# Kernel tuning notes

Measured on AMD Instinct MI355X. Metric: run time of the kernel, lower is better.

Reference implementation:

```python
import jax, jax.numpy as jnp
import numpy as np

S, B, D, H = 1024, 8, 256, 8
DH = D // H
N = S * B
E = 262144
EPS = 1e-5


def setup_inputs():
    key = jax.random.key(0)
    ks = jax.random.split(key, 10)
    g = lambda k, shp, s=0.05: jax.random.normal(k, shp, jnp.float32) * s
    return {
        "x": g(ks[0], (S, B, D), 1.0),
        "condition": g(ks[1], (S, B, 1), 1.0),
        "in_proj_w": g(ks[2], (3 * D, D)),
        "in_proj_b": jnp.zeros((3 * D,), jnp.float32),
        "out_proj_w": g(ks[3], (D, D)),
        "out_proj_b": jnp.zeros((D,), jnp.float32),
        "g1": jnp.ones((D,), jnp.float32), "be1": jnp.zeros((D,), jnp.float32),
        "g2": jnp.ones((D,), jnp.float32), "be2": jnp.zeros((D,), jnp.float32),
        "g3": jnp.ones((D,), jnp.float32), "be3": jnp.zeros((D,), jnp.float32),
        "lin_w": g(ks[4], (D, D)),
        "att_src": g(ks[5], (H, DH)),
        "att_dst": g(ks[6], (H, DH)),
        "gat_bias": jnp.zeros((D,), jnp.float32),
        "w1": g(ks[7], (4 * D, D + 1)),
        "bf1": jnp.zeros((4 * D,), jnp.float32),
        "w2": g(ks[8], (D, 4 * D)),
        "bf2": jnp.zeros((D,), jnp.float32),
        "edge_index": jax.random.randint(ks[9], (2, E), 0, N, jnp.int32),
    }


def _ln(x, g, b):
    m = jnp.mean(x, axis=-1, keepdims=True)
    v = jnp.mean((x - m) ** 2, axis=-1, keepdims=True)
    return (x - m) * jax.lax.rsqrt(v + EPS) * g + b


def _forward(x, condition, in_proj_w, in_proj_b, out_proj_w, out_proj_b,
             g1, be1, g2, be2, g3, be3, lin_w, att_src, att_dst, gat_bias,
             w1, bf1, w2, bf2, edge_index):
    # ---- self-attention (torch MHA, seq-major [S,B,D]) ----
    qkv = jnp.einsum('sbd,ed->sbe', x, in_proj_w) + in_proj_b
    q, k, v = jnp.split(qkv, 3, axis=-1)
    q = q.reshape(S, B, H, DH)
    k = k.reshape(S, B, H, DH)
    v = v.reshape(S, B, H, DH)
    scores = jnp.einsum('sbhd,tbhd->bhst', q, k) / np.float32(np.sqrt(DH))
    a = jax.nn.softmax(scores, axis=-1)
    ctx = jnp.einsum('bhst,tbhd->sbhd', a, v).reshape(S, B, D)
    attn_out = ctx @ out_proj_w.T + out_proj_b
    x1 = _ln(x + attn_out, g1, be1)
    # ---- GATConv over flattened (batch-major) nodes ----
    xr = x1.transpose(1, 0, 2).reshape(N, D)          # node i = b*S + s
    xh = (xr @ lin_w.T).reshape(N, H, DH)
    loops = jnp.arange(N, dtype=edge_index.dtype)     # PyG add_self_loops=True
    src = jnp.concatenate([edge_index[0], loops])
    dst = jnp.concatenate([edge_index[1], loops])
    a_src = jnp.sum(xh * att_src, axis=-1)            # [N,H]
    a_dst = jnp.sum(xh * att_dst, axis=-1)
    e = jax.nn.leaky_relu(a_src[src] + a_dst[dst], 0.2)  # [Et,H]
    m = jax.ops.segment_max(e, dst, num_segments=N)
    ee = jnp.exp(e - m[dst])
    z = jax.ops.segment_sum(ee, dst, num_segments=N)
    alpha = ee / z[dst]
    msg = xh[src] * alpha[:, :, None]                 # [Et,H,DH]
    gout = jax.ops.segment_sum(msg, dst, num_segments=N).reshape(N, D) + gat_bias
    gout = gout.reshape(B, S, D).transpose(1, 0, 2)
    x2 = _ln(x1 + gout, g2, be2)
    # ---- conditioned FFN ----
    xc = jnp.concatenate([x2, condition], axis=-1)    # [S,B,D+1]
    h = jax.nn.relu(xc @ w1.T + bf1)
    f = h @ w2.T + bf2
    return _ln(x2 + f, g3, be3)


def reference(x, condition, in_proj_w, in_proj_b, out_proj_w, out_proj_b,
              g1, be1, g2, be2, g3, be3, lin_w, att_src, att_dst, gat_bias,
              w1, bf1, w2, bf2, edge_index):
    return _forward(x, condition, in_proj_w, in_proj_b, out_proj_w, out_proj_b,
                    g1, be1, g2, be2, g3, be3, lin_w, att_src, att_dst, gat_bias,
                    w1, bf1, w2, bf2, edge_index)
```

## Files before the change

### kernel.cpp

```cpp
#include <hip/hip_runtime.h>
#include <hip/hip_bf16.h>

#define S_ 1024
#define B_ 8
#define D_ 256
#define H_ 8
#define DH_ 32
#define N_ 8192
#define E_ 262144
#define ET_ 270336

typedef unsigned short u16;
typedef float f32x4 __attribute__((ext_vector_type(4)));
typedef __bf16 bf16x8 __attribute__((ext_vector_type(8)));
typedef short s16x4 __attribute__((ext_vector_type(4)));

#define QK_SCALE 0.17677669529663687f

__device__ inline u16 f2bf(float v) {
    unsigned int u = __float_as_uint(v);
    u = (u + 0x7fffu + ((u >> 16) & 1u)) >> 16;
    return (u16)u;
}
__device__ inline float bf2f(u16 u) { return __uint_as_float(((unsigned int)u) << 16); }

__device__ inline unsigned int pack_trunc(float lo, float hi) {
    return __builtin_amdgcn_perm(__float_as_uint(hi), __float_as_uint(lo), 0x07060302u);
}

__device__ inline void gload16(const u16* g, u16* l) {
    __builtin_amdgcn_global_load_lds((const __attribute__((address_space(1))) unsigned int*)g,
                                     (__attribute__((address_space(3))) unsigned int*)l, 16, 0, 0);
}

__device__ inline f32x4 mfma16bf(s16x4 a, s16x4 b, f32x4 c) {
#if __has_builtin(__builtin_amdgcn_mfma_f32_16x16x16bf16_1k)
    return __builtin_amdgcn_mfma_f32_16x16x16bf16_1k(a, b, c, 0, 0, 0);
#else
    asm volatile("v_mfma_f32_16x16x16_bf16 %0, %1, %2, %0" : "+v"(c) : "v"(a), "v"(b));
    return c;
#endif
}

__global__ __launch_bounds__(256) void convert_all(const float* __restrict__ x,  const float* __restrict__ wi,
                                                   const float* __restrict__ wo, const float* __restrict__ wl,
                                                   const float* __restrict__ w1, const float* __restrict__ w2,
                                                   u16* __restrict__ Xbf, u16* __restrict__ Wi, u16* __restrict__ Wo,
                                                   u16* __restrict__ Wl, u16* __restrict__ W1, u16* __restrict__ W2,
                                                   int* __restrict__ count, int* __restrict__ cursor)
{
    const int idx = blockIdx.x * 256 + threadIdx.x;
    const int C0 = 2097152;
    const int C1 = C0 + 196608;
    const int C2 = C1 + 65536;
    const int C3 = C2 + 65536;
    const int C4 = C3 + 294912;
    const int C5 = C4 + 262144;
    const int C6 = C5 + 16384;
    if (idx < C0)      { Xbf[idx] = f2bf(x[idx]); }
    else if (idx < C1) { int i = idx - C0; Wi[i] = f2bf(wi[i]); }
    else if (idx < C2) { int i = idx - C1; Wo[i] = f2bf(wo[i]); }
    else if (idx < C3) { int i = idx - C2; Wl[i] = f2bf(wl[i]); }
    else if (idx < C4) { int i = idx - C3; int r = i / 288, k = i - r * 288;
                         W1[i] = (k < 257) ? f2bf(w1[r * 257 + k]) : (u16)0; }
    else if (idx < C5) { int i = idx - C4; W2[i] = f2bf(w2[i]); }
    else if (idx < C6) { int i = idx - C5; if (i < 8192) count[i] = 0; else cursor[i - 8192] = 0; }
}

template<int BN, int OUTMODE, bool RELU>
__global__ __launch_bounds__(256) void gemm_a16(const u16* __restrict__ A, int lda,
                                                const u16* __restrict__ W, int ldw,
                                                const float* __restrict__ bias,
                                                void* __restrict__ Cv, int ldc, int Ksz)
{
    constexpr int NF = BN / 32;
    __shared__ u16 As[2][128 * 32];
    __shared__ u16 Bs[2][BN * 32];
    const int tid = threadIdx.x;
    const int m0 = blockIdx.y * 128, n0 = blockIdx.x * BN;
    const int lane = tid & 63, w = tid >> 6;
    const int wm = w >> 1, wn = w & 1;
    const int lr = lane & 15, lg = lane >> 4;

    f32x4 acc[4][NF] = {};

    const u16* Ag = A + (size_t)(m0 + (tid >> 2)) * lda + (tid & 3) * 8;
    const u16* Wg = W + (size_t)(n0 + (tid >> 2)) * ldw + (tid & 3) * 8;

    auto stage = [&](int buf, int k0) {
        gload16(Ag + k0,                      &As[buf][tid * 8]);
        gload16(Ag + (size_t)64 * lda + k0,   &As[buf][64 * 32 + tid * 8]);
        gload16(Wg + k0,                      &Bs[buf][tid * 8]);
        if constexpr (BN == 128)
            gload16(Wg + (size_t)64 * ldw + k0, &Bs[buf][64 * 32 + tid * 8]);
    };

    stage(0, 0);
    __syncthreads();
    const int nt = Ksz >> 5;
    int cur = 0;
    for (int kt = 0; kt < nt; ++kt) {
        if (kt + 1 < nt) stage(cur ^ 1, (kt + 1) << 5);
        bf16x8 af[4], bg[NF];
        #pragma unroll
        for (int i = 0; i < 4; ++i)  af[i] = *(const bf16x8*)&As[cur][(wm * 64 + i * 16 + lr) * 32 + lg * 8];
        #pragma unroll
        for (int i = 0; i < NF; ++i) bg[i] = *(const bf16x8*)&Bs[cur][(wn * (BN / 2) + i * 16 + lr) * 32 + lg * 8];
        #pragma unroll
        for (int mi = 0; mi < 4; ++mi)
            #pragma unroll
            for (int ni = 0; ni < NF; ++ni)
                acc[mi][ni] = __builtin_amdgcn_mfma_f32_16x16x32_bf16(af[mi], bg[ni], acc[mi][ni], 0, 0, 0);
        __syncthreads();
        cur ^= 1;
    }
    #pragma unroll
    for (int mi = 0; mi < 4; ++mi)
        #pragma unroll
        for (int ni = 0; ni < NF; ++ni) {
            const int col = n0 + wn * (BN / 2) + ni * 16 + lr;
            const float bv = bias ? bias[col] : 0.f;
            #pragma unroll
            for (int r = 0; r < 4; ++r) {
                const int row = m0 + wm * 64 + mi * 16 + lg * 4 + r;
                float v = acc[mi][ni][r] + bv;
                if (RELU) v = fmaxf(v, 0.f);
                if constexpr (OUTMODE == 1) ((u16*)Cv)[(size_t)row * ldc + col] = f2bf(v);
                else {
                    const int part = col >> 8, hh = (col >> 5) & 7, dh = col & 31;
                    const int ss = row >> 3, bb = row & 7;
                    ((u16*)Cv)[(((size_t)((part * 8 + bb) * 8 + hh)) * 1024 + ss) * 32 + dh] = f2bf(v);
                }
            }
        }
}

template<int MODE>
__global__ __launch_bounds__(512) void gemm_ln(const u16* __restrict__ A, int lda,
                                               const u16* __restrict__ W, int ldw, int Ksz,
                                               const float* __restrict__ bias,
                                               const float* __restrict__ resid,
                                               const float* __restrict__ gamma,
                                               const float* __restrict__ beta,
                                               const float* __restrict__ att_s,
                                               const float* __restrict__ att_d,
                                               float* __restrict__ outf,
                                               u16* __restrict__ outn,
                                               float* __restrict__ asrc,
                                               float* __restrict__ adst)
{
    constexpr int BM = 32;
    __shared__ u16 As[2][BM * 32];
    __shared__ u16 Bs[2][256 * 32];
    __shared__ float2 red[BM][8];
    const int tid = threadIdx.x;
    const int m0 = blockIdx.x * BM;
    const int lane = tid & 63, w = tid >> 6;
    const int rw = w >> 2, cw = w & 3;
    const int lr = lane & 15, lg = lane >> 4;

    f32x4 acc[4] = {};

    auto stage = [&](int buf, int k0) {
        #pragma unroll
        for (int j = 0; j < 2; ++j) {
            const int idx = tid + j * 512;
            gload16(W + (size_t)(idx >> 2) * ldw + (idx & 3) * 8 + k0, &Bs[buf][idx * 8]);
        }
        if (tid < BM * 4)
            gload16(A + (size_t)(m0 + (tid >> 2)) * lda + (tid & 3) * 8 + k0, &As[buf][tid * 8]);
    };
    stage(0, 0);
    __syncthreads();
    const int nt = Ksz >> 5;
    int cur = 0;
    for (int kt = 0; kt < nt; ++kt) {
        if (kt + 1 < nt) stage(cur ^ 1, (kt + 1) << 5);
        bf16x8 af = *(const bf16x8*)&As[cur][(rw * 16 + lr) * 32 + lg * 8];
        bf16x8 bg[4];
        #pragma unroll
        for (int i = 0; i < 4; ++i)  bg[i] = *(const bf16x8*)&Bs[cur][(cw * 64 + i * 16 + lr) * 32 + lg * 8];
        #pragma unroll
        for (int ni = 0; ni < 4; ++ni)
            acc[ni] = __builtin_amdgcn_mfma_f32_16x16x32_bf16(af, bg[ni], acc[ni], 0, 0, 0);
        __syncthreads();
        cur ^= 1;
    }
    int col[4]; float gam[4], bet[4], bv[4], asv[4], adv[4];
    #pragma unroll
    for (int ni = 0; ni < 4; ++ni) {
        col[ni] = cw * 64 + ni * 16 + lr;
        if (MODE != 1) { gam[ni] = gamma[col[ni]]; bet[ni] = beta[col[ni]]; bv[ni] = bias[col[ni]]; }
        else           { asv[ni] = att_s[col[ni]]; adv[ni] = att_d[col[ni]]; }
    }
    #pragma unroll
    for (int r = 0; r < 4; ++r) {
        const int row = rw * 16 + lg * 4 + r;
        const int grow = m0 + row;
        float s1 = 0.f, s2 = 0.f;
        float2 sp0 = {0.f, 0.f}, sp1 = {0.f, 0.f};
        #pragma unroll
        for (int ni = 0; ni < 4; ++ni) {
            float v = acc[ni][r];
            if (MODE != 1) v += bv[ni] + resid[(size_t)grow * 256 + col[ni]];
            acc[ni][r] = v;
            if (MODE == 1) {
                if (ni < 2) { sp0.x += v * asv[ni]; sp0.y += v * adv[ni]; }
                else        { sp1.x += v * asv[ni]; sp1.y += v * adv[ni]; }
            } else { s1 += v; s2 += v * v; }
        }
        #pragma unroll
        for (int msk = 1; msk < 16; msk <<= 1) {
            if (MODE == 1) {
                sp0.x += __shfl_xor(sp0.x, msk, 64); sp0.y += __shfl_xor(sp0.y, msk, 64);
                sp1.x += __shfl_xor(sp1.x, msk, 64); sp1.y += __shfl_xor(sp1.y, msk, 64);
            } else { s1 += __shfl_xor(s1, msk, 64); s2 += __shfl_xor(s2, msk, 64); }
        }
        if (lr == 0) {
            if (MODE == 1) { red[row][cw * 2] = sp0; red[row][cw * 2 + 1] = sp1; }
            else           { red[row][cw] = (float2){s1, s2}; }
        }
    }
    __syncthreads();
    if (MODE == 1) {
        #pragma unroll
        for (int r = 0; r < 4; ++r) {
            const int grow = m0 + rw * 16 + lg * 4 + r;
            #pragma unroll
            for (int ni = 0; ni < 4; ++ni)
                outn[(size_t)grow * 256 + col[ni]] = f2bf(acc[ni][r]);
        }
        for (int idx = tid; idx < BM * 8; idx += 512) {
            const int row = idx >> 3, h = idx & 7;
            asrc[(size_t)(m0 + row) * 8 + h] = red[row][h].x;
            adst[(size_t)(m0 + row) * 8 + h] = red[row][h].y;
        }
    } else {
        #pragma unroll
        for (int r = 0; r < 4; ++r) {
            const int row = rw * 16 + lg * 4 + r;
            const int grow = m0 + row;
            const float2 t0 = red[row][0], t1 = red[row][1], t2 = red[row][2], t3 = red[row][3];
            const float mean = (t0.x + t1.x + t2.x + t3.x) * (1.f / 256.f);
            const float var  = (t0.y + t1.y + t2.y + t3.y) * (1.f / 256.f) - mean * mean;
            const float rs = rsqrtf(var + 1e-5f);
            #pragma unroll
            for (int ni = 0; ni < 4; ++ni) {
                const float o = (acc[ni][r] - mean) * rs * gam[ni] + bet[ni];
                outf[(size_t)grow * 256 + col[ni]] = o;
                if (MODE == 0) {
                    const int node = (grow & 7) * 1024 + (grow >> 3);
                    outn[(size_t)node * 256 + col[ni]] = f2bf(o);
                }
            }
        }
    }
}

__global__ __launch_bounds__(512) void attn_mfma(const u16* __restrict__ qkv, u16* __restrict__ ctx)
{
    const int qt = blockIdx.x, bh = blockIdx.y;
    const int b = bh >> 3, h = bh & 7;
    const int tid = threadIdx.x, lane = tid & 63, w = tid >> 6;
    const int c = lane & 15, g = lane >> 4;

    __shared__ __align__(16) u16 Ks[128][40];
    __shared__ __align__(16) u16 Vt[32][132];

    const size_t plane = (size_t)(b * 8 + h) * 32768;
    const int q0 = qt * 128 + w * 16;
    const bf16x8 qf = *(const bf16x8*)&qkv[plane + (size_t)(q0 + c) * 32 + g * 8];
    const u16* kbase = qkv + 2097152 + plane;

    float m = -1e30f, l = 0.f;
    f32x4 o0 = {}, o1 = {};

    for (int kt = 0; kt < 8; ++kt) {
        const int t0 = kt * 128;
        __syncthreads();
        {
            const int r = tid >> 2, c0 = (tid & 3) * 8;
            const u16* kp = kbase + (size_t)(t0 + r) * 32 + c0;
            *(uint4*)&Ks[r][c0] = *(const uint4*)kp;
            u16 vb[8];
            *(uint4*)vb = *(const uint4*)(kp + 2097152);
            #pragma unroll
            for (int i = 0; i < 8; ++i) Vt[c0 + i][r] = vb[i];
        }
        __syncthreads();
        f32x4 sc[8];
        #pragma unroll
        for (int t = 0; t < 8; ++t) {
            const bf16x8 kf = *(const bf16x8*)&Ks[t * 16 + c][g * 8];
            sc[t] = __builtin_amdgcn_mfma_f32_16x16x32_bf16(kf, qf, (f32x4){0.f, 0.f, 0.f, 0.f}, 0, 0, 0);
        }
        float tm = sc[0][0];
        #pragma unroll
        for (int t = 0; t < 8; ++t)
            #pragma unroll
            for (int r = 0; r < 4; ++r) tm = fmaxf(tm, sc[t][r]);
        tm = fmaxf(tm, __shfl_xor(tm, 16, 64));
        tm = fmaxf(tm, __shfl_xor(tm, 32, 64));
        const float mn = fmaxf(m, tm);
        const float sf = __expf((m - mn) * QK_SCALE);
        m = mn;
        l *= sf; o0 *= sf; o1 *= sf;
        unsigned int pb[8][2];
        float ls = 0.f;
        #pragma unroll
        for (int t = 0; t < 8; ++t) {
            const float p0 = __expf((sc[t][0] - m) * QK_SCALE);
            const float p1 = __expf((sc[t][1] - m) * QK_SCALE);
            const float p2 = __expf((sc[t][2] - m) * QK_SCALE);
            const float p3 = __expf((sc[t][3] - m) * QK_SCALE);
            ls += (p0 + p1) + (p2 + p3);
            pb[t][0] = pack_trunc(p0, p1);
            pb[t][1] = pack_trunc(p2, p3);
        }
        l += ls;
        #pragma unroll
        for (int t = 0; t < 8; ++t) {
            union { unsigned int u[2]; s16x4 v; } pu;
            pu.u[0] = pb[t][0]; pu.u[1] = pb[t][1];
            const s16x4 vf0 = *(const s16x4*)&Vt[c][t * 16 + g * 4];
            const s16x4 vf1 = *(const s16x4*)&Vt[16 + c][t * 16 + g * 4];
            o0 = mfma16bf(vf0, pu.v, o0);
            o1 = mfma16bf(vf1, pu.v, o1);
        }
    }
    l += __shfl_xor(l, 16, 64);
    l += __shfl_xor(l, 32, 64);
    const float inv = 1.f / l;
    u16 ob[8];
    #pragma unroll
    for (int r = 0; r < 4; ++r) { ob[r] = f2bf(o0[r] * inv); ob[4 + r] = f2bf(o1[r] * inv); }
    const size_t obase = ((size_t)(q0 + c) * 8 + b) * 256 + h * 32 + g * 4;
    *(uint2*)&ctx[obase]      = *(uint2*)ob;
    *(uint2*)&ctx[obase + 16] = *(uint2*)(ob + 4);
}

__global__ __launch_bounds__(256) void edge_hist(const int* __restrict__ ei, int* __restrict__ count)
{
    int e = blockIdx.x * 256 + threadIdx.x;
    if (e >= ET_) return;
    int dst = (e < E_) ? ei[E_ + e] : e - E_;
    atomicAdd(&count[dst], 1);
}

__global__ __launch_bounds__(1024) void scan_offsets(const int* __restrict__ count, int* __restrict__ offset)
{
    __shared__ int s[1024];
    const int t = threadIdx.x;
    const int base = t * 8;
    int c[8]; int sum = 0;
    #pragma unroll
    for (int i = 0; i < 8; ++i) { c[i] = count[base + i]; sum += c[i]; }
    s[t] = sum; __syncthreads();
    for (int off = 1; off < 1024; off <<= 1) {
        int add = (t >= off) ? s[t - off] : 0;
        __syncthreads();
        s[t] += add;
        __syncthreads();
    }
    int run = (t == 0) ? 0 : s[t - 1];
    #pragma unroll
    for (int i = 0; i < 8; ++i) { offset[base + i] = run; run += c[i]; }
    if (t == 1023) offset[8192] = run;
}

__global__ __launch_bounds__(256) void edge_scatter(const int* __restrict__ ei, const int* __restrict__ offset,
                                                    int* __restrict__ cursor, int* __restrict__ sorted)
{
    int e = blockIdx.x * 256 + threadIdx.x;
    if (e >= ET_) return;
    int src, dst;
    if (e < E_) { src = ei[e]; dst = ei[E_ + e]; }
    else        { src = dst = e - E_; }
    int pos = offset[dst] + atomicAdd(&cursor[dst], 1);
    sorted[pos] = src;
}

__global__ __launch_bounds__(256) void gat_gather_ln(const int* __restrict__ sorted, const int* __restrict__ offset,
                                                     const float* __restrict__ asrc, const float* __restrict__ adst,
                                                     const u16* __restrict__ xh,
                                                     const float* __restrict__ X1f, const float* __restrict__ gb,
                                                     const float* __restrict__ g2, const float* __restrict__ be2,
                                                     const float* __restrict__ cond,
                                                     float* __restrict__ X2f, u16* __restrict__ X2pad)
{
    const int wid = threadIdx.x >> 6, lane = threadIdx.x & 63;
    const int pair = wid >> 1, half = wid & 1;
    const int dst = blockIdx.x * 2 + pair;
    const int h = lane >> 3;
    const float ad = adst[dst * 8 + h];
    const int beg = offset[dst], end = offset[dst + 1];
    const int mid = beg + ((end - beg + 1) >> 1);
    const int b0 = half ? mid : beg;
    const int b1 = half ? end : mid;

    __shared__ float szs[2][8];
    __shared__ __align__(16) float sa[2][64][4];

    float z = 0.f, a0 = 0.f, a1 = 0.f, a2 = 0.f, a3 = 0.f;
    #pragma unroll 4
    for (int i = b0; i < b1; ++i) {
        const int src = sorted[i];
        float e = asrc[src * 8 + h] + ad;
        e = fmaxf(e, 0.2f * e);
        const float p = __expf(e);
        z += p;
        const uint2 xv = *(const uint2*)&xh[(size_t)src * 256 + lane * 4];
        a0 += p * __uint_as_float(xv.x << 16);
        a1 += p * __uint_as_float(xv.x & 0xffff0000u);
        a2 += p * __uint_as_float(xv.y << 16);
        a3 += p * __uint_as_float(xv.y & 0xffff0000u);
    }
    if (half) {
        if ((lane & 7) == 0) szs[pair][h] = z;
        *(f32x4*)&sa[pair][lane][0] = (f32x4){a0, a1, a2, a3};
    }
    __syncthreads();
    if (half) return;
    const f32x4 ap = *(const f32x4*)&sa[pair][lane][0];
    const float zt = z + szs[pair][h];
    const float inv = 1.f / zt;
    const int row = (dst & 1023) * 8 + (dst >> 10);
    f32x4 v = *(const f32x4*)&X1f[(size_t)row * 256 + lane * 4];
    const f32x4 bb = *(const f32x4*)&gb[lane * 4];
    v[0] += (a0 + ap[0]) * inv + bb[0];
    v[1] += (a1 + ap[1]) * inv + bb[1];
    v[2] += (a2 + ap[2]) * inv + bb[2];
    v[3] += (a3 + ap[3]) * inv + bb[3];
    float s1 = (v[0] + v[1]) + (v[2] + v[3]);
    float s2 = (v[0] * v[0] + v[1] * v[1]) + (v[2] * v[2] + v[3] * v[3]);
    #pragma unroll
    for (int msk = 1; msk < 64; msk <<= 1) { s1 += __shfl_xor(s1, msk, 64); s2 += __shfl_xor(s2, msk, 64); }
    const float mean = s1 * (1.f / 256.f);
    const float var = s2 * (1.f / 256.f) - mean * mean;
    const float rs = rsqrtf(var + 1e-5f);
    const f32x4 gg = *(const f32x4*)&g2[lane * 4];
    const f32x4 be = *(const f32x4*)&be2[lane * 4];
    f32x4 o;
    u16 ob[4];
    #pragma unroll
    for (int i = 0; i < 4; ++i) { o[i] = (v[i] - mean) * rs * gg[i] + be[i]; ob[i] = f2bf(o[i]); }
    *(f32x4*)&X2f[(size_t)row * 256 + lane * 4] = o;
    *(uint2*)&X2pad[(size_t)row * 288 + lane * 4] = *(uint2*)ob;
    if (lane < 8) {
        u16 zz[4] = {0, 0, 0, 0};
        if (lane == 0) zz[0] = f2bf(cond[row]);
        *(uint2*)&X2pad[(size_t)row * 288 + 256 + lane * 4] = *(uint2*)zz;
    }
}

extern "C" void kernel_launch(void* const* d_in, const int* in_sizes, int n_in,
                              void* d_out, int out_size, void* d_ws, size_t ws_size,
                              hipStream_t stream)
{
    const float* x          = (const float*)d_in[0];
    const float* condition  = (const float*)d_in[1];
    const float* in_proj_w  = (const float*)d_in[2];
    const float* in_proj_b  = (const float*)d_in[3];
    const float* out_proj_w = (const float*)d_in[4];
    const float* out_proj_b = (const float*)d_in[5];
    const float* g1         = (const float*)d_in[6];
    const float* be1        = (const float*)d_in[7];
    const float* g2         = (const float*)d_in[8];
    const float* be2        = (const float*)d_in[9];
    const float* g3         = (const float*)d_in[10];
    const float* be3        = (const float*)d_in[11];
    const float* lin_w      = (const float*)d_in[12];
    const float* att_src    = (const float*)d_in[13];
    const float* att_dst    = (const float*)d_in[14];
    const float* gat_bias   = (const float*)d_in[15];
    const float* w1         = (const float*)d_in[16];
    const float* bf1        = (const float*)d_in[17];
    const float* w2         = (const float*)d_in[18];
    const float* bf2        = (const float*)d_in[19];
    const int*   edge_index = (const int*)d_in[20];
    float* out = (float*)d_out;

    char* ws = (char*)d_ws;
    u16*   QKV    = (u16*)(ws + 0);
    u16*   Hb     = (u16*)(ws + 0);
    u16*   CTX    = (u16*)(ws + 16777216);
    u16*   X1node = (u16*)(ws + 20971520);
    u16*   XH     = (u16*)(ws + 25165824);
    float* X1f    = (float*)(ws + 29360128);
    float* X2f    = (float*)(ws + 37748736);
    u16*   X2pad  = (u16*)(ws + 46137344);
    u16*   Xbf    = (u16*)(ws + 50855936);
    float* ASRC   = (float*)(ws + 55050240);
    float* ADST   = (float*)(ws + 55312384);
    u16*   W_inp  = (u16*)(ws + 55574528);
    u16*   W_out  = (u16*)(ws + 55967744);
    u16*   W_lin  = (u16*)(ws + 56098816);
    u16*   W_w1   = (u16*)(ws + 56229888);
    u16*   W_w2   = (u16*)(ws + 56819712);
    int*   COUNT  = (int*)(ws + 57344000);
    int*   OFFSET = (int*)(ws + 57376768);
    int*   CURSOR = (int*)(ws + 57413632);
    int*   SORTED = (int*)(ws + 57446400);

    convert_all<<<11712, 256, 0, stream>>>(x, in_proj_w, out_proj_w, lin_w, w1, w2,
                                           Xbf, W_inp, W_out, W_lin, W_w1, W_w2, COUNT, CURSOR);
    edge_hist<<<1056, 256, 0, stream>>>(edge_index, COUNT);
    scan_offsets<<<1, 1024, 0, stream>>>(COUNT, OFFSET);
    edge_scatter<<<1056, 256, 0, stream>>>(edge_index, OFFSET, CURSOR, SORTED);
    gemm_a16<64, 2, false><<<dim3(12, 64), 256, 0, stream>>>(Xbf, 256, W_inp, 256, in_proj_b, QKV, 768, 256);
    attn_mfma<<<dim3(8, 64), 512, 0, stream>>>(QKV, CTX);
    gemm_ln<0><<<256, 512, 0, stream>>>(CTX, 256, W_out, 256, 256, out_proj_b, x, g1, be1,
                                        nullptr, nullptr, X1f, X1node, nullptr, nullptr);
    gemm_ln<1><<<256, 512, 0, stream>>>(X1node, 256, W_lin, 256, 256, nullptr, nullptr, nullptr, nullptr,
                                        att_src, att_dst, nullptr, XH, ASRC, ADST);
    gat_gather_ln<<<4096, 256, 0, stream>>>(SORTED, OFFSET, ASRC, ADST, XH,
                                            X1f, gat_bias, g2, be2, condition, X2f, X2pad);
    gemm_a16<128, 1, true><<<dim3(8, 64), 256, 0, stream>>>(X2pad, 288, W_w1, 288, bf1, Hb, 1024, 288);
    gemm_ln<2><<<256, 512, 0, stream>>>(Hb, 1024, W_w2, 1024, 1024, bf2, X2f, g3, be3,
                                        nullptr, nullptr, out, nullptr, nullptr, nullptr);
}
```

Before: 157.5 us.

## Fold edge sort stages into GEMM and attention launches, double-buffer attention K/V

The separate edge histogram, scan and scatter kernels are removed. Their work now runs as extra blocks appended to the QKV GEMM, the attention kernel and the out-proj GEMM+LN launch, which cuts three kernel launches and lets the small graph-preprocessing work overlap with the dense compute. The attention kernel also double-buffers its K/V shared-memory tiles so the next tile loads while the current one is computed. The generic GEMM template is split into specialised kernels with fixed sizes. The costs are extra blocks in each grid, a scan reduced to a single 512-thread block, and more shared memory in the attention kernel.

```diff
diff --git a/kernel.cpp b/kernel.cpp
--- a/kernel.cpp
+++ b/kernel.cpp
@@ -67,49 +67,50 @@
     else if (idx < C6) { int i = idx - C5; if (i < 8192) count[i] = 0; else cursor[i - 8192] = 0; }
 }
 
-template<int BN, int OUTMODE, bool RELU>
-__global__ __launch_bounds__(256) void gemm_a16(const u16* __restrict__ A, int lda,
-                                                const u16* __restrict__ W, int ldw,
-                                                const float* __restrict__ bias,
-                                                void* __restrict__ Cv, int ldc, int Ksz)
-{
-    constexpr int NF = BN / 32;
+__global__ __launch_bounds__(256) void gemm_qkv_hist(const u16* __restrict__ A,
+                                                     const u16* __restrict__ W,
+                                                     const float* __restrict__ bias,
+                                                     u16* __restrict__ Cv,
+                                                     const int* __restrict__ ei, int* __restrict__ count)
+{
+    const int tid = threadIdx.x;
+    if (blockIdx.x >= 768) {
+        const int e = (blockIdx.x - 768) * 256 + tid;
+        const int dst = (e < E_) ? ei[E_ + e] : e - E_;
+        atomicAdd(&count[dst], 1);
+        return;
+    }
     __shared__ u16 As[2][128 * 32];
-    __shared__ u16 Bs[2][BN * 32];
-    const int tid = threadIdx.x;
-    const int m0 = blockIdx.y * 128, n0 = blockIdx.x * BN;
+    __shared__ u16 Bs[2][64 * 32];
+    const int m0 = (blockIdx.x / 12) * 128, n0 = (blockIdx.x % 12) * 64;
     const int lane = tid & 63, w = tid >> 6;
     const int wm = w >> 1, wn = w & 1;
     const int lr = lane & 15, lg = lane >> 4;
 
-    f32x4 acc[4][NF] = {};
-
-    const u16* Ag = A + (size_t)(m0 + (tid >> 2)) * lda + (tid & 3) * 8;
-    const u16* Wg = W + (size_t)(n0 + (tid >> 2)) * ldw + (tid & 3) * 8;
+    f32x4 acc[4][2] = {};
+
+    const u16* Ag = A + (size_t)(m0 + (tid >> 2)) * 256 + (tid & 3) * 8;
+    const u16* Wg = W + (size_t)(n0 + (tid >> 2)) * 256 + (tid & 3) * 8;
 
     auto stage = [&](int buf, int k0) {
-        gload16(Ag + k0,                      &As[buf][tid * 8]);
-        gload16(Ag + (size_t)64 * lda + k0,   &As[buf][64 * 32 + tid * 8]);
-        gload16(Wg + k0,                      &Bs[buf][tid * 8]);
-        if constexpr (BN == 128)
-            gload16(Wg + (size_t)64 * ldw + k0, &Bs[buf][64 * 32 + tid * 8]);
+        gload16(Ag + k0,                    &As[buf][tid * 8]);
+        gload16(Ag + (size_t)64 * 256 + k0, &As[buf][64 * 32 + tid * 8]);
+        gload16(Wg + k0,                    &Bs[buf][tid * 8]);
     };
-
     stage(0, 0);
     __syncthreads();
-    const int nt = Ksz >> 5;
     int cur = 0;
-    for (int kt = 0; kt < nt; ++kt) {
-        if (kt + 1 < nt) stage(cur ^ 1, (kt + 1) << 5);
-        bf16x8 af[4], bg[NF];
-        #pragma unroll
-        for (int i = 0; i < 4; ++i)  af[i] = *(const bf16x8*)&As[cur][(wm * 64 + i * 16 + lr) * 32 + lg * 8];
-        #pragma unroll
-        for (int i = 0; i < NF; ++i) bg[i] = *(const bf16x8*)&Bs[cur][(wn * (BN / 2) + i * 16 + lr) * 32 + lg * 8];
+    for (int kt = 0; kt < 8; ++kt) {
+        if (kt + 1 < 8) stage(cur ^ 1, (kt + 1) << 5);
+        bf16x8 af[4], bg[2];
+        #pragma unroll
+        for (int i = 0; i < 4; ++i) af[i] = *(const bf16x8*)&As[cur][(wm * 64 + i * 16 + lr) * 32 + lg * 8];
+        #pragma unroll
+        for (int i = 0; i < 2; ++i) bg[i] = *(const bf16x8*)&Bs[cur][(wn * 32 + i * 16 + lr) * 32 + lg * 8];
         #pragma unroll
         for (int mi = 0; mi < 4; ++mi)
             #pragma unroll
-            for (int ni = 0; ni < NF; ++ni)
+            for (int ni = 0; ni < 2; ++ni)
                 acc[mi][ni] = __builtin_amdgcn_mfma_f32_16x16x32_bf16(af[mi], bg[ni], acc[mi][ni], 0, 0, 0);
         __syncthreads();
         cur ^= 1;
@@ -117,22 +118,124 @@
     #pragma unroll
     for (int mi = 0; mi < 4; ++mi)
         #pragma unroll
-        for (int ni = 0; ni < NF; ++ni) {
-            const int col = n0 + wn * (BN / 2) + ni * 16 + lr;
-            const float bv = bias ? bias[col] : 0.f;
+        for (int ni = 0; ni < 2; ++ni) {
+            const int col = n0 + wn * 32 + ni * 16 + lr;
+            const float bv = bias[col];
+            const int part = col >> 8, hh = (col >> 5) & 7, dh = col & 31;
             #pragma unroll
             for (int r = 0; r < 4; ++r) {
                 const int row = m0 + wm * 64 + mi * 16 + lg * 4 + r;
-                float v = acc[mi][ni][r] + bv;
-                if (RELU) v = fmaxf(v, 0.f);
-                if constexpr (OUTMODE == 1) ((u16*)Cv)[(size_t)row * ldc + col] = f2bf(v);
-                else {
-                    const int part = col >> 8, hh = (col >> 5) & 7, dh = col & 31;
-                    const int ss = row >> 3, bb = row & 7;
-                    ((u16*)Cv)[(((size_t)((part * 8 + bb) * 8 + hh)) * 1024 + ss) * 32 + dh] = f2bf(v);
-                }
+                const int ss = row >> 3, bb = row & 7;
+                Cv[(((size_t)((part * 8 + bb) * 8 + hh)) * 1024 + ss) * 32 + dh] = f2bf(acc[mi][ni][r] + bv);
             }
         }
+}
+
+__global__ __launch_bounds__(512) void attn_mfma(const u16* __restrict__ qkv, u16* __restrict__ ctx,
+                                                 const int* __restrict__ count, int* __restrict__ offset)
+{
+    const int tid = threadIdx.x;
+    if (blockIdx.x == 512) {
+        __shared__ int s[512];
+        const int base = tid * 16;
+        int c[16]; int sum = 0;
+        #pragma unroll
+        for (int i = 0; i < 16; ++i) { c[i] = count[base + i]; sum += c[i]; }
+        s[tid] = sum; __syncthreads();
+        for (int off = 1; off < 512; off <<= 1) {
+            int add = (tid >= off) ? s[tid - off] : 0;
+            __syncthreads();
+            s[tid] += add;
+            __syncthreads();
+        }
+        int run = (tid == 0) ? 0 : s[tid - 1];
+        #pragma unroll
+        for (int i = 0; i < 16; ++i) { offset[base + i] = run; run += c[i]; }
+        if (tid == 511) offset[8192] = run;
+        return;
+    }
+    const int qt = blockIdx.x & 7, bh = blockIdx.x >> 3;
+    const int b = bh >> 3, h = bh & 7;
+    const int lane = tid & 63, w = tid >> 6;
+    const int c = lane & 15, g = lane >> 4;
+
+    __shared__ __align__(16) u16 Ks[2][128][40];
+    __shared__ __align__(16) u16 Vt[2][32][132];
+
+    const size_t plane = (size_t)(b * 8 + h) * 32768;
+    const int q0 = qt * 128 + w * 16;
+    const bf16x8 qf = *(const bf16x8*)&qkv[plane + (size_t)(q0 + c) * 32 + g * 8];
+    const u16* kbase = qkv + 2097152 + plane;
+
+    auto stage = [&](int buf, int kt) {
+        const int r = tid >> 2, c0 = (tid & 3) * 8;
+        const u16* kp = kbase + (size_t)(kt * 128 + r) * 32 + c0;
+        *(uint4*)&Ks[buf][r][c0] = *(const uint4*)kp;
+        u16 vb[8];
+        *(uint4*)vb = *(const uint4*)(kp + 2097152);
+        #pragma unroll
+        for (int i = 0; i < 8; ++i) Vt[buf][c0 + i][r] = vb[i];
+    };
+
+    float m = -1e30f, l = 0.f;
+    f32x4 o0 = {}, o1 = {};
+
+    stage(0, 0);
+    __syncthreads();
+    int cur = 0;
+    for (int kt = 0; kt < 8; ++kt) {
+        if (kt + 1 < 8) stage(cur ^ 1, kt + 1);
+        f32x4 sc[8];
+        #pragma unroll
+        for (int t = 0; t < 8; ++t) {
+            const bf16x8 kf = *(const bf16x8*)&Ks[cur][t * 16 + c][g * 8];
+            sc[t] = __builtin_amdgcn_mfma_f32_16x16x32_bf16(kf, qf, (f32x4){0.f, 0.f, 0.f, 0.f}, 0, 0, 0);
+        }
+        float tm = sc[0][0];
+        #pragma unroll
+        for (int t = 0; t < 8; ++t)
+            #pragma unroll
+            for (int r = 0; r < 4; ++r) tm = fmaxf(tm, sc[t][r]);
+        tm = fmaxf(tm, __shfl_xor(tm, 16, 64));
+        tm = fmaxf(tm, __shfl_xor(tm, 32, 64));
+        const float mn = fmaxf(m, tm);
+        const float sf = __expf((m - mn) * QK_SCALE);
+        m = mn;
+        l *= sf; o0 *= sf; o1 *= sf;
+        unsigned int pb[8][2];
+        float ls = 0.f;
+        #pragma unroll
+        for (int t = 0; t < 8; ++t) {
+            const float p0 = __expf((sc[t][0] - m) * QK_SCALE);
+            const float p1 = __expf((sc[t][1] - m) * QK_SCALE);
+            const float p2 = __expf((sc[t][2] - m) * QK_SCALE);
+            const float p3 = __expf((sc[t][3] - m) * QK_SCALE);
+            ls += (p0 + p1) + (p2 + p3);
+            pb[t][0] = pack_trunc(p0, p1);
+            pb[t][1] = pack_trunc(p2, p3);
+        }
+        l += ls;
+        #pragma unroll
+        for (int t = 0; t < 8; ++t) {
+            union { unsigned int u[2]; s16x4 v; } pu;
+            pu.u[0] = pb[t][0]; pu.u[1] = pb[t][1];
+            const s16x4 vf0 = *(const s16x4*)&Vt[cur][c][t * 16 + g * 4];
+            const s16x4 vf1 = *(const s16x4*)&Vt[cur][16 + c][t * 16 + g * 4];
+            o0 = mfma16bf(vf0, pu.v, o0);
+            o1 = mfma16bf(vf1, pu.v, o1);
+        }
+        __syncthreads();
+        cur ^= 1;
+    }
+    l += __shfl_xor(l, 16, 64);
+    l += __shfl_xor(l, 32, 64);
+    const float inv = 1.f / l;
+    u16 ob[8];
+    #pragma unroll
+    for (int r = 0; r < 4; ++r) { ob[r] = f2bf(o0[r] * inv); ob[4 + r] = f2bf(o1[r] * inv); }
+    const size_t obase = ((size_t)(q0 + c) * 8 + b) * 256 + h * 32 + g * 4;
+    *(uint2*)&ctx[obase]      = *(uint2*)ob;
+    *(uint2*)&ctx[obase + 16] = *(uint2*)(ob + 4);
 }
 
 template<int MODE>
@@ -147,13 +250,26 @@
                                                float* __restrict__ outf,
                                                u16* __restrict__ outn,
                                                float* __restrict__ asrc,
-                                               float* __restrict__ adst)
+                                               float* __restrict__ adst,
+                                               const int* __restrict__ ei,
+                                               const int* __restrict__ offset,
+                                               int* __restrict__ cursor,
+                                               int* __restrict__ sorted)
 {
     constexpr int BM = 32;
+    const int tid = threadIdx.x;
+    if (MODE == 0 && blockIdx.x >= 256) {
+        const int e = (blockIdx.x - 256) * 512 + tid;
+        int src, dst;
+        if (e < E_) { src = ei[e]; dst = ei[E_ + e]; }
+        else        { src = dst = e - E_; }
+        const int pos = offset[dst] + atomicAdd(&cursor[dst], 1);
+        sorted[pos] = src;
+        return;
+    }
     __shared__ u16 As[2][BM * 32];
     __shared__ u16 Bs[2][256 * 32];
     __shared__ float2 red[BM][8];
-    const int tid = threadIdx.x;
     const int m0 = blockIdx.x * BM;
     const int lane = tid & 63, w = tid >> 6;
     const int rw = w >> 2, cw = w & 3;
@@ -255,129 +371,6 @@
             }
         }
     }
-}
-
-__global__ __launch_bounds__(512) void attn_mfma(const u16* __restrict__ qkv, u16* __restrict__ ctx)
-{
-    const int qt = blockIdx.x, bh = blockIdx.y;
-    const int b = bh >> 3, h = bh & 7;
-    const int tid = threadIdx.x, lane = tid & 63, w = tid >> 6;
-    const int c = lane & 15, g = lane >> 4;
-
-    __shared__ __align__(16) u16 Ks[128][40];
-    __shared__ __align__(16) u16 Vt[32][132];
-
-    const size_t plane = (size_t)(b * 8 + h) * 32768;
-    const int q0 = qt * 128 + w * 16;
-    const bf16x8 qf = *(const bf16x8*)&qkv[plane + (size_t)(q0 + c) * 32 + g * 8];
-    const u16* kbase = qkv + 2097152 + plane;
-
-    float m = -1e30f, l = 0.f;
-    f32x4 o0 = {}, o1 = {};
-
-    for (int kt = 0; kt < 8; ++kt) {
-        const int t0 = kt * 128;
-        __syncthreads();
-        {
-            const int r = tid >> 2, c0 = (tid & 3) * 8;
-            const u16* kp = kbase + (size_t)(t0 + r) * 32 + c0;
-            *(uint4*)&Ks[r][c0] = *(const uint4*)kp;
-            u16 vb[8];
-            *(uint4*)vb = *(const uint4*)(kp + 2097152);
-            #pragma unroll
-            for (int i = 0; i < 8; ++i) Vt[c0 + i][r] = vb[i];
-        }
-        __syncthreads();
-        f32x4 sc[8];
-        #pragma unroll
-        for (int t = 0; t < 8; ++t) {
-            const bf16x8 kf = *(const bf16x8*)&Ks[t * 16 + c][g * 8];
-            sc[t] = __builtin_amdgcn_mfma_f32_16x16x32_bf16(kf, qf, (f32x4){0.f, 0.f, 0.f, 0.f}, 0, 0, 0);
-        }
-        float tm = sc[0][0];
-        #pragma unroll
-        for (int t = 0; t < 8; ++t)
-            #pragma unroll
-            for (int r = 0; r < 4; ++r) tm = fmaxf(tm, sc[t][r]);
-        tm = fmaxf(tm, __shfl_xor(tm, 16, 64));
-        tm = fmaxf(tm, __shfl_xor(tm, 32, 64));
-        const float mn = fmaxf(m, tm);
-        const float sf = __expf((m - mn) * QK_SCALE);
-        m = mn;
-        l *= sf; o0 *= sf; o1 *= sf;
-        unsigned int pb[8][2];
-        float ls = 0.f;
-        #pragma unroll
-        for (int t = 0; t < 8; ++t) {
-            const float p0 = __expf((sc[t][0] - m) * QK_SCALE);
-            const float p1 = __expf((sc[t][1] - m) * QK_SCALE);
-            const float p2 = __expf((sc[t][2] - m) * QK_SCALE);
-            const float p3 = __expf((sc[t][3] - m) * QK_SCALE);
-            ls += (p0 + p1) + (p2 + p3);
-            pb[t][0] = pack_trunc(p0, p1);
-            pb[t][1] = pack_trunc(p2, p3);
-        }
-        l += ls;
-        #pragma unroll
-        for (int t = 0; t < 8; ++t) {
-            union { unsigned int u[2]; s16x4 v; } pu;
-            pu.u[0] = pb[t][0]; pu.u[1] = pb[t][1];
-            const s16x4 vf0 = *(const s16x4*)&Vt[c][t * 16 + g * 4];
-            const s16x4 vf1 = *(const s16x4*)&Vt[16 + c][t * 16 + g * 4];
-            o0 = mfma16bf(vf0, pu.v, o0);
-            o1 = mfma16bf(vf1, pu.v, o1);
-        }
-    }
-    l += __shfl_xor(l, 16, 64);
-    l += __shfl_xor(l, 32, 64);
-    const float inv = 1.f / l;
-    u16 ob[8];
-    #pragma unroll
-    for (int r = 0; r < 4; ++r) { ob[r] = f2bf(o0[r] * inv); ob[4 + r] = f2bf(o1[r] * inv); }
-    const size_t obase = ((size_t)(q0 + c) * 8 + b) * 256 + h * 32 + g * 4;
-    *(uint2*)&ctx[obase]      = *(uint2*)ob;
-    *(uint2*)&ctx[obase + 16] = *(uint2*)(ob + 4);
-}
-
-__global__ __launch_bounds__(256) void edge_hist(const int* __restrict__ ei, int* __restrict__ count)
-{
-    int e = blockIdx.x * 256 + threadIdx.x;
-    if (e >= ET_) return;
-    int dst = (e < E_) ? ei[E_ + e] : e - E_;
-    atomicAdd(&count[dst], 1);
-}
-
-__global__ __launch_bounds__(1024) void scan_offsets(const int* __restrict__ count, int* __restrict__ offset)
-{
-    __shared__ int s[1024];
-    const int t = threadIdx.x;
-    const int base = t * 8;
-    int c[8]; int sum = 0;
-    #pragma unroll
-    for (int i = 0; i < 8; ++i) { c[i] = count[base + i]; sum += c[i]; }
-    s[t] = sum; __syncthreads();
-    for (int off = 1; off < 1024; off <<= 1) {
-        int add = (t >= off) ? s[t - off] : 0;
-        __syncthreads();
-        s[t] += add;
-        __syncthreads();
-    }
-    int run = (t == 0) ? 0 : s[t - 1];
-    #pragma unroll
-    for (int i = 0; i < 8; ++i) { offset[base + i] = run; run += c[i]; }
-    if (t == 1023) offset[8192] = run;
-}
-
-__global__ __launch_bounds__(256) void edge_scatter(const int* __restrict__ ei, const int* __restrict__ offset,
-                                                    int* __restrict__ cursor, int* __restrict__ sorted)
-{
-    int e = blockIdx.x * 256 + threadIdx.x;
-    if (e >= ET_) return;
-    int src, dst;
-    if (e < E_) { src = ei[e]; dst = ei[E_ + e]; }
-    else        { src = dst = e - E_; }
-    int pos = offset[dst] + atomicAdd(&cursor[dst], 1);
-    sorted[pos] = src;
 }
 
 __global__ __launch_bounds__(256) void gat_gather_ln(const int* __restrict__ sorted, const int* __restrict__ offset,
@@ -451,6 +444,63 @@
         if (lane == 0) zz[0] = f2bf(cond[row]);
         *(uint2*)&X2pad[(size_t)row * 288 + 256 + lane * 4] = *(uint2*)zz;
     }
+}
+
+__global__ __launch_bounds__(256) void gemm_w1(const u16* __restrict__ A,
+                                               const u16* __restrict__ W,
+                                               const float* __restrict__ bias,
+                                               u16* __restrict__ Cv)
+{
+    __shared__ u16 As[2][128 * 32];
+    __shared__ u16 Bs[2][128 * 32];
+    const int tid = threadIdx.x;
+    const int m0 = blockIdx.y * 128, n0 = blockIdx.x * 128;
+    const int lane = tid & 63, w = tid >> 6;
+    const int wm = w >> 1, wn = w & 1;
+    const int lr = lane & 15, lg = lane >> 4;
+
+    f32x4 acc[4][4] = {};
+
+    const u16* Ag = A + (size_t)(m0 + (tid >> 2)) * 288 + (tid & 3) * 8;
+    const u16* Wg = W + (size_t)(n0 + (tid >> 2)) * 288 + (tid & 3) * 8;
+
+    auto stage = [&](int buf, int k0) {
+        gload16(Ag + k0,                    &As[buf][tid * 8]);
+        gload16(Ag + (size_t)64 * 288 + k0, &As[buf][64 * 32 + tid * 8]);
+        gload16(Wg + k0,                    &Bs[buf][tid * 8]);
+        gload16(Wg + (size_t)64 * 288 + k0, &Bs[buf][64 * 32 + tid * 8]);
+    };
+    stage(0, 0);
+    __syncthreads();
+    int cur = 0;
+    for (int kt = 0; kt < 9; ++kt) {
+        if (kt + 1 < 9) stage(cur ^ 1, (kt + 1) << 5);
+        bf16x8 af[4], bg[4];
+        #pragma unroll
+        for (int i = 0; i < 4; ++i) {
+            af[i] = *(const bf16x8*)&As[cur][(wm * 64 + i * 16 + lr) * 32 + lg * 8];
+            bg[i] = *(const bf16x8*)&Bs[cur][(wn * 64 + i * 16 + lr) * 32 + lg * 8];
+        }
+        #pragma unroll
+        for (int mi = 0; mi < 4; ++mi)
+            #pragma unroll
+            for (int ni = 0; ni < 4; ++ni)
+                acc[mi][ni] = __builtin_amdgcn_mfma_f32_16x16x32_bf16(af[mi], bg[ni], acc[mi][ni], 0, 0, 0);
+        __syncthreads();
+        cur ^= 1;
+    }
+    #pragma unroll
+    for (int mi = 0; mi < 4; ++mi)
+        #pragma unroll
+        for (int ni = 0; ni < 4; ++ni) {
+            const int col = n0 + wn * 64 + ni * 16 + lr;
+            const float bv = bias[col];
+            #pragma unroll
+            for (int r = 0; r < 4; ++r) {
+                const int row = m0 + wm * 64 + mi * 16 + lg * 4 + r;
+                Cv[(size_t)row * 1024 + col] = f2bf(fmaxf(acc[mi][ni][r] + bv, 0.f));
+            }
+        }
 }
 
 extern "C" void kernel_launch(void* const* d_in, const int* in_sizes, int n_in,
@@ -504,18 +554,18 @@
 
     convert_all<<<11712, 256, 0, stream>>>(x, in_proj_w, out_proj_w, lin_w, w1, w2,
                                            Xbf, W_inp, W_out, W_lin, W_w1, W_w2, COUNT, CURSOR);
-    edge_hist<<<1056, 256, 0, stream>>>(edge_index, COUNT);
-    scan_offsets<<<1, 1024, 0, stream>>>(COUNT, OFFSET);
-    edge_scatter<<<1056, 256, 0, stream>>>(edge_index, OFFSET, CURSOR, SORTED);
-    gemm_a16<64, 2, false><<<dim3(12, 64), 256, 0, stream>>>(Xbf, 256, W_inp, 256, in_proj_b, QKV, 768, 256);
-    attn_mfma<<<dim3(8, 64), 512, 0, stream>>>(QKV, CTX);
-    gemm_ln<0><<<256, 512, 0, stream>>>(CTX, 256, W_out, 256, 256, out_proj_b, x, g1, be1,
-                                        nullptr, nullptr, X1f, X1node, nullptr, nullptr);
+    gemm_qkv_hist<<<1824, 256, 0, stream>>>(Xbf, W_inp, in_proj_b, QKV, edge_index, COUNT);
+    attn_mfma<<<513, 512, 0, stream>>>(QKV, CTX, COUNT, OFFSET);
+    gemm_ln<0><<<784, 512, 0, stream>>>(CTX, 256, W_out, 256, 256, out_proj_b, x, g1, be1,
+                                        nullptr, nullptr, X1f, X1node, nullptr, nullptr,
+                                        edge_index, OFFSET, CURSOR, SORTED);
     gemm_ln<1><<<256, 512, 0, stream>>>(X1node, 256, W_lin, 256, 256, nullptr, nullptr, nullptr, nullptr,
-                                        att_src, att_dst, nullptr, XH, ASRC, ADST);
+                                        att_src, att_dst, nullptr, XH, ASRC, ADST,
+                                        nullptr, nullptr, nullptr, nullptr);
     gat_gather_ln<<<4096, 256, 0, stream>>>(SORTED, OFFSET, ASRC, ADST, XH,
                                             X1f, gat_bias, g2, be2, condition, X2f, X2pad);
-    gemm_a16<128, 1, true><<<dim3(8, 64), 256, 0, stream>>>(X2pad, 288, W_w1, 288, bf1, Hb, 1024, 288);
+    gemm_w1<<<dim3(8, 64), 256, 0, stream>>>(X2pad, W_w1, bf1, Hb);
     gemm_ln<2><<<256, 512, 0, stream>>>(Hb, 1024, W_w2, 1024, 1024, bf2, X2f, g3, be3,
-                                        nullptr, nullptr, out, nullptr, nullptr, nullptr);
-}
+                                        nullptr, nullptr, out, nullptr, nullptr, nullptr,
+                                        nullptr, nullptr, nullptr, nullptr);
+}
```

Result: faster. 143.1 us (-9.2%).
